# Kernel tuning notes

Hardware: AMD Instinct MI355X
Metric: run time of the kernel (lower is better)

The kernel has to match this reference:

```python
import jax, jax.numpy as jnp
import numpy as np

# dims: V vocab, D embed, C classes, S seq, L layers, M proj_dim (random features), B batch
V, D, C, S, L, M, B = 32000, 512, 2, 2048, 4, 64, 16
H = 4 * D  # FFN hidden


def setup_inputs() -> dict:
    key = jax.random.key(0)
    ks = jax.random.split(key, 16)
    sc = 0.02
    n = lambda k, shape, s=sc: jax.random.normal(k, shape, jnp.float32) * s
    return {
        'x': jax.random.randint(ks[0], (B, S), 0, V),
        'embed': n(ks[1], (V, D)),
        'pos': n(ks[2], (S, D)),
        'Wq': n(ks[3], (L, D, D)), 'bq': jnp.zeros((L, D), jnp.float32),
        'Wk': n(ks[4], (L, D, D)), 'bk': jnp.zeros((L, D), jnp.float32),
        'Wv': n(ks[5], (L, D, D)), 'bv': jnp.zeros((L, D), jnp.float32),
        'P': jax.random.normal(ks[6], (L, D, M), jnp.float32) / np.sqrt(D),  # Performer random-feature projection
        'Wo': n(ks[7], (L, D, D)), 'bo': jnp.zeros((L, D), jnp.float32),
        'ln_g': jnp.ones((L, D), jnp.float32), 'ln_b': jnp.zeros((L, D), jnp.float32),
        'W1': n(ks[8], (L, D, H)), 'b1': jnp.zeros((L, H), jnp.float32),
        'W2': n(ks[9], (L, H, D)), 'b2': jnp.zeros((L, D), jnp.float32),
        'Wc1': n(ks[10], (D, D // 2)), 'bc1': jnp.zeros((D // 2,), jnp.float32),
        'Wc2': n(ks[11], (D // 2, C)), 'bc2': jnp.zeros((C,), jnp.float32),
    }


def _layernorm(x, g, b, eps=1e-5):
    mu = x.mean(-1, keepdims=True)
    var = ((x - mu) ** 2).mean(-1, keepdims=True)
    return (x - mu) * jax.lax.rsqrt(var + eps) * g + b


def reference(x, embed, pos, Wq, bq, Wk, bk, Wv, bv, P, Wo, bo,
              ln_g, ln_b, W1, b1, W2, b2, Wc1, bc1, Wc2, bc2):
    # token embedding + learned positional embedding
    h = embed[x] + pos[None, :, :]  # [B,S,D]
    for l in range(L):
        r = h
        # Performer linear attention
        q = h @ Wq[l] + bq[l]
        k = h @ Wk[l] + bk[l]
        v = h @ Wv[l] + bv[l]
        pq = jax.nn.elu(q @ P[l]) + 1.0  # [B,S,M] positive feature map
        pk = jax.nn.elu(k @ P[l]) + 1.0
        kv = jnp.einsum('bsm,bsd->bmd', pk, v)              # associative K^T V reduction
        z = jnp.einsum('bsm,bm->bs', pq, pk.sum(axis=1)) + 1e-6
        att = jnp.einsum('bsm,bmd->bsd', pq, kv) / z[..., None]
        att = att @ Wo[l] + bo[l]
        # LayerNorm -> FFN (dropout is identity in eval)
        hn = _layernorm(att, ln_g[l], ln_b[l])
        ff = jax.nn.gelu(hn @ W1[l] + b1[l], approximate=False) @ W2[l] + b2[l]
        h = ff + r  # residual around the whole Sequential block
    pooled = h[:, 0, :]  # CLS pooling
    hid = jax.nn.relu(pooled @ Wc1 + bc1)
    return hid @ Wc2 + bc2  # [B,C] logits
```

## Files before the change

kernel.cpp:

```cpp
#include <hip/hip_runtime.h>
#include <hip/hip_bf16.h>
#include <math.h>

constexpr int kV = 32000;
constexpr int kD = 512;
constexpr int kC = 2;
constexpr int kS = 2048;
constexpr int kL = 4;
constexpr int kM = 64;
constexpr int kB = 16;
constexpr int kH = 2048;
constexpr int kBS = kB * kS;

typedef __hip_bfloat16 bf16;
using bf16x8 = __attribute__((ext_vector_type(8))) short;
using f32x4  = __attribute__((ext_vector_type(4))) float;

#define GLOBAL_LOAD_LDS16(gp, lp)                                              \
  __builtin_amdgcn_global_load_lds(                                            \
      (const __attribute__((address_space(1))) void*)(gp),                     \
      (__attribute__((address_space(3))) void*)(lp), 16, 0, 0)

__device__ inline unsigned short f2bf_u16(float f) {
  bf16 b = __float2bfloat16(f);
  return *reinterpret_cast<unsigned short*>(&b);
}

__global__ __launch_bounds__(256) void embed_kernel(const int* __restrict__ x,
    const float* __restrict__ emb, const float* __restrict__ pos,
    float* __restrict__ h, bf16* __restrict__ hb) {
  int tid = blockIdx.x * 256 + threadIdx.x;
  int row = tid >> 7;
  int d4  = tid & 127;
  int tok = x[row];
  int s   = row & (kS - 1);
  float4 e = ((const float4*)emb)[(size_t)tok * 128 + d4];
  float4 p = ((const float4*)pos)[(size_t)s * 128 + d4];
  float4 o;
  o.x = e.x + p.x; o.y = e.y + p.y; o.z = e.z + p.z; o.w = e.w + p.w;
  ((float4*)h)[(size_t)row * 128 + d4] = o;
  ushort4 ub;
  ub.x = f2bf_u16(o.x); ub.y = f2bf_u16(o.y);
  ub.z = f2bf_u16(o.z); ub.w = f2bf_u16(o.w);
  ((ushort4*)hb)[(size_t)row * 128 + d4] = ub;
}

__global__ __launch_bounds__(256) void transpose_cast_kernel(
    const float* __restrict__ W, bf16* __restrict__ Wt, int K, int N,
    size_t zsW, size_t zsWt) {
  __shared__ float tile[32][33];
  W  += zsW  * blockIdx.z;
  Wt += zsWt * blockIdx.z;
  const int k0 = blockIdx.x * 32, n0 = blockIdx.y * 32;
  int tx = threadIdx.x & 31, ty = threadIdx.x >> 5;
#pragma unroll
  for (int i = 0; i < 32; i += 8)
    tile[ty + i][tx] = W[(size_t)(k0 + ty + i) * N + n0 + tx];
  __syncthreads();
#pragma unroll
  for (int i = 0; i < 32; i += 8)
    Wt[(size_t)(n0 + ty + i) * K + k0 + tx] = __float2bfloat16(tile[tx][ty + i]);
}

__global__ __launch_bounds__(256) void cast_bf16_kernel(
    const float* __restrict__ src, bf16* __restrict__ dst) {
  int gid = blockIdx.x * 256 + threadIdx.x;
  float4 v = ((const float4*)src)[gid];
  ushort4 u;
  u.x = f2bf_u16(v.x); u.y = f2bf_u16(v.y);
  u.z = f2bf_u16(v.z); u.w = f2bf_u16(v.w);
  ((ushort4*)dst)[gid] = u;
}

__global__ __launch_bounds__(256) void zero512_kernel(float* __restrict__ p) {
  if (threadIdx.x < 128) ((float4*)p)[threadIdx.x] = make_float4(0.f, 0.f, 0.f, 0.f);
}

__global__ __launch_bounds__(256) void wfold_dual_kernel(
    const float* __restrict__ Wq, const float* __restrict__ Wk,
    const float* __restrict__ P, bf16* __restrict__ Wqpt,
    bf16* __restrict__ Wkpt) {
  int gid = blockIdx.x * 256 + threadIdx.x;
  int l   = gid >> 16;
  int id  = gid & 65535;
  const float* Pl = P + (size_t)l * kD * kM;
  const float* W  = ((id < 32768) ? Wq : Wk) + (size_t)l * kD * kD;
  bf16* out       = ((id < 32768) ? Wqpt : Wkpt) + (size_t)l * kM * kD;
  id &= 32767;
  int m  = id & 63;
  int kk = id >> 6;
  float a0 = 0.f, a1 = 0.f, a2 = 0.f, a3 = 0.f;
#pragma unroll 4
  for (int c = 0; c < kD; c += 4) {
    float4 w = *(const float4*)&W[(size_t)kk * kD + c];
    a0 = fmaf(w.x, Pl[(size_t)(c + 0) * kM + m], a0);
    a1 = fmaf(w.y, Pl[(size_t)(c + 1) * kM + m], a1);
    a2 = fmaf(w.z, Pl[(size_t)(c + 2) * kM + m], a2);
    a3 = fmaf(w.w, Pl[(size_t)(c + 3) * kM + m], a3);
  }
  out[(size_t)m * kD + kk] = __float2bfloat16((a0 + a1) + (a2 + a3));
}

__global__ __launch_bounds__(512) void bfold_kernel(const float* __restrict__ bq,
    const float* __restrict__ bk, const float* __restrict__ P,
    float* __restrict__ bqp, float* __restrict__ bkp) {
  int l = threadIdx.x >> 7;
  int t = threadIdx.x & 127;
  int m = t & (kM - 1);
  const float* Pl  = P + (size_t)l * kD * kM;
  const float* src = ((t >> 6) ? bk : bq) + (size_t)l * kD;
  float* dst       = ((t >> 6) ? bkp : bqp) + (size_t)l * kM;
  float acc = 0.f;
  for (int c = 0; c < kD; ++c) acc += src[c] * Pl[(size_t)c * kM + m];
  dst[m] = acc;
}

__global__ __launch_bounds__(256) void bvwo_kernel(const float* __restrict__ bv,
    const float* __restrict__ Wo, float* __restrict__ bvWo) {
  __shared__ float part[4][64];
  int l = blockIdx.y;
  bv   += (size_t)l * kD;
  Wo   += (size_t)l * kD * kD;
  bvWo += (size_t)l * kD;
  int d0 = blockIdx.x * 64;
  int dc = threadIdx.x & 63;
  int eg = threadIdx.x >> 6;
  float acc = 0.f;
  int e0 = eg * 128;
#pragma unroll 4
  for (int e = e0; e < e0 + 128; ++e)
    acc = fmaf(bv[e], Wo[(size_t)e * kD + d0 + dc], acc);
  part[eg][dc] = acc;
  __syncthreads();
  if (eg == 0)
    bvWo[d0 + dc] = (part[0][dc] + part[1][dc]) + (part[2][dc] + part[3][dc]);
}

template <int BK, int BN, int ACT, bool HAS_RES, bool HAS_OUTER, bool WRITE_F32, bool WRITE_BF16>
__global__ __launch_bounds__(256) void mfma_gemm(
    const bf16* __restrict__ A, const bf16* __restrict__ Wt,
    const float* __restrict__ bias, const float* __restrict__ rowv,
    const float* __restrict__ colv, const float* __restrict__ res,
    float* __restrict__ C, bf16* __restrict__ Cb,
    size_t zsA, size_t zsB, size_t zsC, int K, int N) {
  constexpr int NJ = BN / 32;
  constexpr int CPR = BK / 8;
  constexpr int SW = (BK == 32) ? 1 : 0;
  __shared__ short As[128 * BK];
  __shared__ short Bs[BN * BK];
  A  += zsA * blockIdx.z;
  Wt += zsB * blockIdx.z;
  if (C)  C  += zsC * blockIdx.z;
  if (Cb) Cb += zsC * blockIdx.z;
  const int tid  = threadIdx.x;
  const int lane = tid & 63;
  const int wave = tid >> 6;
  const int nx = gridDim.x;
  const int SH = (gridDim.y & 7) ? gridDim.y : 8;
  const int b_lin = blockIdx.y * nx + blockIdx.x;
  const int stripe = b_lin / (nx * SH);
  const int rem = b_lin - stripe * (nx * SH);
  const int row0 = (stripe * SH + (rem % SH)) * 128;
  const int col0 = (rem / SH) * BN;
  const int wr = (wave & 1) * 64;
  const int wc = (wave >> 1) * (BN / 2);
  const int lcol = lane & 15;
  const int quad = lane >> 4;

  f32x4 acc[4][NJ];
#pragma unroll
  for (int i = 0; i < 4; ++i)
#pragma unroll
    for (int j = 0; j < NJ; ++j) acc[i][j] = (f32x4){0.f, 0.f, 0.f, 0.f};

  for (int k0 = 0; k0 < K; k0 += BK) {
#pragma unroll
    for (int p = 0; p < 128 * CPR / 256; ++p) {
      int idx = p * 256 + tid;
      int r = idx / CPR;
      int kc = (idx % CPR) ^ ((r >> SW) & (CPR - 1));
      GLOBAL_LOAD_LDS16(&A[(size_t)(row0 + r) * K + k0 + kc * 8], &As[idx * 8]);
    }
#pragma unroll
    for (int p = 0; p < BN * CPR / 256; ++p) {
      int idx = p * 256 + tid;
      int r = idx / CPR;
      int kc = (idx % CPR) ^ ((r >> SW) & (CPR - 1));
      GLOBAL_LOAD_LDS16(&Wt[(size_t)(col0 + r) * K + k0 + kc * 8], &Bs[idx * 8]);
    }
    __syncthreads();
#pragma unroll
    for (int kh = 0; kh < BK / 32; ++kh) {
      bf16x8 af[4], bfr[NJ];
#pragma unroll
      for (int i = 0; i < 4; ++i) {
        int rr = wr + i * 16 + lcol;
        int slot = (kh * 4 + quad) ^ ((rr >> SW) & (CPR - 1));
        af[i] = *(const bf16x8*)&As[(rr * CPR + slot) * 8];
      }
#pragma unroll
      for (int j = 0; j < NJ; ++j) {
        int rr = wc + j * 16 + lcol;
        int slot = (kh * 4 + quad) ^ ((rr >> SW) & (CPR - 1));
        bfr[j] = *(const bf16x8*)&Bs[(rr * CPR + slot) * 8];
      }
#pragma unroll
      for (int i = 0; i < 4; ++i)
#pragma unroll
        for (int j = 0; j < NJ; ++j)
          acc[i][j] = __builtin_amdgcn_mfma_f32_16x16x32_bf16(af[i], bfr[j], acc[i][j], 0, 0, 0);
    }
    __syncthreads();
  }

#pragma unroll
  for (int i = 0; i < 4; ++i) {
#pragma unroll
    for (int r = 0; r < 4; ++r) {
      int grow = row0 + wr + i * 16 + quad * 4 + r;
#pragma unroll
      for (int j = 0; j < NJ; ++j) {
        int gcol = col0 + wc + j * 16 + lcol;
        float v = acc[i][j][r];
        if (HAS_OUTER) v += rowv[grow] * colv[gcol];
        else v += bias[gcol];
        if (ACT == 2) v = 0.5f * v * (1.0f + erff(v * 0.70710678118654752f));
        size_t off = (size_t)grow * N + gcol;
        if (HAS_RES) v += res[off];
        if (WRITE_F32) C[off] = v;
        if (WRITE_BF16) Cb[off] = __float2bfloat16(v);
      }
    }
  }
}

template <int ACT, bool HAS_RES, bool WRITE_F32, bool WRITE_BF16>
__global__ __launch_bounds__(512) void mfma_gemm_cnt(
    const bf16* __restrict__ A, const bf16* __restrict__ Wt,
    const float* __restrict__ bias, const float* __restrict__ res,
    float* __restrict__ C, bf16* __restrict__ Cb, int K, int N) {
  constexpr int BK = 64, BN = 128, BM = 128;
  __shared__ short As[2][BM * BK];
  __shared__ short Bs[2][BN * BK];
  const int tid  = threadIdx.x;
  const int lane = tid & 63;
  const int wave = tid >> 6;
  const int nx = gridDim.x;
  const int SH = (gridDim.y & 7) ? gridDim.y : 8;
  const int b_lin = blockIdx.y * nx + blockIdx.x;
  const int stripe = b_lin / (nx * SH);
  const int rem = b_lin - stripe * (nx * SH);
  const int row0 = (stripe * SH + (rem % SH)) * BM;
  const int col0 = (rem / SH) * BN;
  const int wr = (wave & 1) * 64;
  const int wc = (wave >> 1) * 32;
  const int lcol = lane & 15;
  const int quad = lane >> 4;

  f32x4 acc[4][2];
#pragma unroll
  for (int i = 0; i < 4; ++i)
#pragma unroll
    for (int j = 0; j < 2; ++j) acc[i][j] = (f32x4){0.f, 0.f, 0.f, 0.f};

  auto stage = [&](int buf, int k0) {
#pragma unroll
    for (int p = 0; p < 2; ++p) {
      int idx = p * 512 + tid;
      int r = idx >> 3;
      int kc = (idx & 7) ^ (r & 7);
      GLOBAL_LOAD_LDS16(&A[(size_t)(row0 + r) * K + k0 + kc * 8], &As[buf][idx * 8]);
    }
#pragma unroll
    for (int p = 0; p < 2; ++p) {
      int idx = p * 512 + tid;
      int r = idx >> 3;
      int kc = (idx & 7) ^ (r & 7);
      GLOBAL_LOAD_LDS16(&Wt[(size_t)(col0 + r) * K + k0 + kc * 8], &Bs[buf][idx * 8]);
    }
  };

  auto compute = [&](int buf) {
#pragma unroll
    for (int kh = 0; kh < 2; ++kh) {
      bf16x8 af[4], bfr[2];
#pragma unroll
      for (int i = 0; i < 4; ++i) {
        int rr = wr + i * 16 + lcol;
        int slot = (kh * 4 + quad) ^ (rr & 7);
        af[i] = *(const bf16x8*)&As[buf][(rr * 8 + slot) * 8];
      }
#pragma unroll
      for (int j = 0; j < 2; ++j) {
        int rr = wc + j * 16 + lcol;
        int slot = (kh * 4 + quad) ^ (rr & 7);
        bfr[j] = *(const bf16x8*)&Bs[buf][(rr * 8 + slot) * 8];
      }
#pragma unroll
      for (int i = 0; i < 4; ++i)
#pragma unroll
        for (int j = 0; j < 2; ++j)
          acc[i][j] = __builtin_amdgcn_mfma_f32_16x16x32_bf16(af[i], bfr[j], acc[i][j], 0, 0, 0);
    }
  };

  const int NT = K / BK;
  stage(0, 0);
  stage(1, BK);
  for (int t = 0; t < NT - 1; ++t) {
    const int cur = t & 1;
    asm volatile("s_waitcnt vmcnt(4)" ::: "memory");
    __builtin_amdgcn_s_barrier();
    compute(cur);
    __builtin_amdgcn_s_barrier();
    if (t + 2 < NT) stage(cur, (t + 2) * BK);
  }
  asm volatile("s_waitcnt vmcnt(0)" ::: "memory");
  __builtin_amdgcn_s_barrier();
  compute((NT - 1) & 1);

#pragma unroll
  for (int i = 0; i < 4; ++i) {
#pragma unroll
    for (int r = 0; r < 4; ++r) {
      int grow = row0 + wr + i * 16 + quad * 4 + r;
#pragma unroll
      for (int j = 0; j < 2; ++j) {
        int gcol = col0 + wc + j * 16 + lcol;
        float v = acc[i][j][r] + bias[gcol];
        if (ACT == 2) v = 0.5f * v * (1.0f + erff(v * 0.70710678118654752f));
        size_t off = (size_t)grow * N + gcol;
        if (HAS_RES) v += res[off];
        if (WRITE_F32) C[off] = v;
        if (WRITE_BF16) Cb[off] = __float2bfloat16(v);
      }
    }
  }
}

__global__ __launch_bounds__(256) void skinny_dual_gemm(
    const bf16* __restrict__ A, const bf16* __restrict__ Wq,
    const bf16* __restrict__ Wk, const float* __restrict__ bq,
    const float* __restrict__ bk, float* __restrict__ pq,
    float* __restrict__ pk) {
  __shared__ short As[64 * 32];
  __shared__ short Bs[128 * 32];
  const int tid  = threadIdx.x;
  const int lane = tid & 63;
  const int wave = tid >> 6;
  const int row0 = blockIdx.x * 64;
  const int lcol = lane & 15;
  const int quad = lane >> 4;

  f32x4 accq[4], acck[4];
#pragma unroll
  for (int i = 0; i < 4; ++i) {
    accq[i] = (f32x4){0.f, 0.f, 0.f, 0.f};
    acck[i] = (f32x4){0.f, 0.f, 0.f, 0.f};
  }

  for (int k0 = 0; k0 < kD; k0 += 32) {
    {
      int r = tid >> 2;
      int kc = (tid & 3) ^ ((r >> 1) & 3);
      GLOBAL_LOAD_LDS16(&A[(size_t)(row0 + r) * kD + k0 + kc * 8], &As[tid * 8]);
    }
#pragma unroll
    for (int p = 0; p < 2; ++p) {
      int idx = p * 256 + tid;
      int r = idx >> 2;
      int kc = (idx & 3) ^ ((r >> 1) & 3);
      const bf16* src = (r < 64) ? &Wq[(size_t)r * kD + k0 + kc * 8]
                                 : &Wk[(size_t)(r - 64) * kD + k0 + kc * 8];
      GLOBAL_LOAD_LDS16(src, &Bs[idx * 8]);
    }
    __syncthreads();
    bf16x8 af[4], bq_f, bk_f;
#pragma unroll
    for (int i = 0; i < 4; ++i) {
      int rr = i * 16 + lcol;
      af[i] = *(const bf16x8*)&As[(rr * 4 + (quad ^ ((rr >> 1) & 3))) * 8];
    }
    {
      int rr = wave * 16 + lcol;
      bq_f = *(const bf16x8*)&Bs[(rr * 4 + (quad ^ ((rr >> 1) & 3))) * 8];
      int rr2 = 64 + wave * 16 + lcol;
      bk_f = *(const bf16x8*)&Bs[(rr2 * 4 + (quad ^ ((rr2 >> 1) & 3))) * 8];
    }
#pragma unroll
    for (int i = 0; i < 4; ++i) {
      accq[i] = __builtin_amdgcn_mfma_f32_16x16x32_bf16(af[i], bq_f, accq[i], 0, 0, 0);
      acck[i] = __builtin_amdgcn_mfma_f32_16x16x32_bf16(af[i], bk_f, acck[i], 0, 0, 0);
    }
    __syncthreads();
  }

#pragma unroll
  for (int i = 0; i < 4; ++i) {
#pragma unroll
    for (int r = 0; r < 4; ++r) {
      int grow = row0 + i * 16 + quad * 4 + r;
      int gcol = wave * 16 + lcol;
      float vq = accq[i][r] + bq[gcol];
      vq = (vq > 0.f) ? (vq + 1.f) : expf(vq);
      pq[(size_t)grow * kM + gcol] = vq;
      float vk = acck[i][r] + bk[gcol];
      vk = (vk > 0.f) ? (vk + 1.f) : expf(vk);
      pk[(size_t)grow * kM + gcol] = vk;
    }
  }
}

__global__ __launch_bounds__(256) void kvh_split_kernel(const float* __restrict__ pk,
    const bf16* __restrict__ hb, float* __restrict__ part) {
  __shared__ float pkS[16][64];
  __shared__ float vS[16][256];
  const int d0 = blockIdx.x * 256, b = blockIdx.y, split = blockIdx.z;
  const int s_beg = split * 128;
  const float* pkb = pk + (size_t)b * kS * kM;
  const bf16* hbb  = hb + (size_t)b * kS * kD;
  const int tid = threadIdx.x;
  const int tx = tid & 15, ty = tid >> 4;
  float4 acc[4][4];
#pragma unroll
  for (int i = 0; i < 4; ++i)
#pragma unroll
    for (int j = 0; j < 4; ++j) acc[i][j] = make_float4(0.f, 0.f, 0.f, 0.f);

  for (int s0 = s_beg; s0 < s_beg + 128; s0 += 16) {
    {
      int e = tid * 4;
      int sr = e >> 6, mc = e & 63;
      *(float4*)&pkS[sr][mc] = *(const float4*)&pkb[(size_t)(s0 + sr) * kM + mc];
    }
#pragma unroll
    for (int p = 0; p < 2; ++p) {
      int idx = p * 256 + tid;
      int sr = idx >> 5, dc8 = idx & 31;
      uint4 raw = *(const uint4*)&hbb[(size_t)(s0 + sr) * kD + d0 + dc8 * 8];
      float4 f0, f1;
      f0.x = __uint_as_float(raw.x << 16);
      f0.y = __uint_as_float(raw.x & 0xffff0000u);
      f0.z = __uint_as_float(raw.y << 16);
      f0.w = __uint_as_float(raw.y & 0xffff0000u);
      f1.x = __uint_as_float(raw.z << 16);
      f1.y = __uint_as_float(raw.z & 0xffff0000u);
      f1.z = __uint_as_float(raw.w << 16);
      f1.w = __uint_as_float(raw.w & 0xffff0000u);
      *(float4*)&vS[sr][dc8 * 8]     = f0;
      *(float4*)&vS[sr][dc8 * 8 + 4] = f1;
    }
    __syncthreads();
#pragma unroll
    for (int sr = 0; sr < 16; ++sr) {
      float a[4];
#pragma unroll
      for (int i = 0; i < 4; ++i) a[i] = pkS[sr][ty * 4 + i];
      float4 bv4[4];
#pragma unroll
      for (int j = 0; j < 4; ++j) bv4[j] = *(const float4*)&vS[sr][tx * 16 + j * 4];
#pragma unroll
      for (int i = 0; i < 4; ++i)
#pragma unroll
        for (int j = 0; j < 4; ++j) {
          acc[i][j].x += a[i] * bv4[j].x;
          acc[i][j].y += a[i] * bv4[j].y;
          acc[i][j].z += a[i] * bv4[j].z;
          acc[i][j].w += a[i] * bv4[j].w;
        }
    }
    __syncthreads();
  }
  float* pp = part + (((size_t)split * kB + b) * kM) * kD;
#pragma unroll
  for (int i = 0; i < 4; ++i)
#pragma unroll
    for (int j = 0; j < 4; ++j)
      *(float4*)&pp[(size_t)(ty * 4 + i) * kD + d0 + tx * 16 + j * 4] = acc[i][j];
}

__global__ __launch_bounds__(256) void kvh_reduce_kernel(const float* __restrict__ part,
                                                         bf16* __restrict__ kvhb) {
  int gid = blockIdx.x * 256 + threadIdx.x;
  float4 s = make_float4(0.f, 0.f, 0.f, 0.f);
#pragma unroll
  for (int sp = 0; sp < 16; ++sp) {
    float4 p = ((const float4*)part)[(size_t)sp * (kB * kM * kD / 4) + gid];
    s.x += p.x; s.y += p.y; s.z += p.z; s.w += p.w;
  }
  ushort4 u;
  u.x = f2bf_u16(s.x); u.y = f2bf_u16(s.y);
  u.z = f2bf_u16(s.z); u.w = f2bf_u16(s.w);
  ((ushort4*)kvhb)[gid] = u;
}

__global__ __launch_bounds__(256) void zero_pks_kernel(float* __restrict__ p) {
  ((float4*)p)[threadIdx.x] = make_float4(0.f, 0.f, 0.f, 0.f);
}

__global__ __launch_bounds__(256) void pksum_kernel(const float* __restrict__ pk,
                                                    float* __restrict__ pksum) {
  __shared__ float part[4][64];
  int b = blockIdx.x >> 4;
  int split = blockIdx.x & 15;
  int lane = threadIdx.x & 63, w = threadIdx.x >> 6;
  float s = 0.f;
  int base = split * 128 + w * 32;
  for (int i = 0; i < 32; ++i)
    s += pk[((size_t)b * kS + base + i) * kM + lane];
  part[w][lane] = s;
  __syncthreads();
  if (w == 0)
    atomicAdd(&pksum[b * kM + lane],
              part[0][lane] + part[1][lane] + part[2][lane] + part[3][lane]);
}

__global__ __launch_bounds__(256) void att_ln_kernel(
    const float* __restrict__ pq, const float* __restrict__ kvo,
    const float* __restrict__ pks, const float* __restrict__ bo,
    const float* __restrict__ g, const float* __restrict__ bb,
    bf16* __restrict__ out) {
  __shared__ float pqS[32][68];
  __shared__ float kvS[16][520];
  const int s0 = blockIdx.x * 32, b = blockIdx.y;
  const int tid = threadIdx.x;
  const int tx = tid & 15, ty = tid >> 4;

#pragma unroll
  for (int i = 0; i < 2; ++i) {
    int f4 = tid + i * 256;
    int r = f4 >> 4, c = (f4 & 15) * 4;
    *(float4*)&pqS[r][c] = *(const float4*)&pq[((size_t)(b * kS + s0 + r)) * kM + c];
  }

  float4 acc[2][8];
#pragma unroll
  for (int i = 0; i < 2; ++i)
#pragma unroll
    for (int j = 0; j < 8; ++j) acc[i][j] = make_float4(0.f, 0.f, 0.f, 0.f);

  for (int m0 = 0; m0 < kM; m0 += 16) {
#pragma unroll
    for (int p = 0; p < 8; ++p) {
      int idx = p * 256 + tid;
      int sr = idx >> 7, c4 = idx & 127;
      *(float4*)&kvS[sr][c4 * 4] =
          *(const float4*)&kvo[((size_t)b * kM + m0 + sr) * kD + c4 * 4];
    }
    __syncthreads();
#pragma unroll
    for (int mm = 0; mm < 16; ++mm) {
      float a0 = pqS[ty * 2 + 0][m0 + mm];
      float a1 = pqS[ty * 2 + 1][m0 + mm];
#pragma unroll
      for (int j = 0; j < 8; ++j) {
        float4 bv = *(const float4*)&kvS[mm][j * 64 + tx * 4];
        acc[0][j].x += a0 * bv.x; acc[0][j].y += a0 * bv.y;
        acc[0][j].z += a0 * bv.z; acc[0][j].w += a0 * bv.w;
        acc[1][j].x += a1 * bv.x; acc[1][j].y += a1 * bv.y;
        acc[1][j].z += a1 * bv.z; acc[1][j].w += a1 * bv.w;
      }
    }
    __syncthreads();
  }

  float4 pk4 = *(const float4*)&pks[b * kM + tx * 4];
  float z0 = pqS[ty * 2 + 0][tx * 4 + 0] * pk4.x + pqS[ty * 2 + 0][tx * 4 + 1] * pk4.y +
             pqS[ty * 2 + 0][tx * 4 + 2] * pk4.z + pqS[ty * 2 + 0][tx * 4 + 3] * pk4.w;
  float z1 = pqS[ty * 2 + 1][tx * 4 + 0] * pk4.x + pqS[ty * 2 + 1][tx * 4 + 1] * pk4.y +
             pqS[ty * 2 + 1][tx * 4 + 2] * pk4.z + pqS[ty * 2 + 1][tx * 4 + 3] * pk4.w;
  z0 += __shfl_xor(z0, 1); z0 += __shfl_xor(z0, 2);
  z0 += __shfl_xor(z0, 4); z0 += __shfl_xor(z0, 8);
  z1 += __shfl_xor(z1, 1); z1 += __shfl_xor(z1, 2);
  z1 += __shfl_xor(z1, 4); z1 += __shfl_xor(z1, 8);
  float zi0 = 1.0f / (z0 + 1e-6f);
  float zi1 = 1.0f / (z1 + 1e-6f);

#pragma unroll
  for (int j = 0; j < 8; ++j) {
    float4 bo4 = *(const float4*)&bo[j * 64 + tx * 4];
    acc[0][j].x = acc[0][j].x * zi0 + bo4.x; acc[0][j].y = acc[0][j].y * zi0 + bo4.y;
    acc[0][j].z = acc[0][j].z * zi0 + bo4.z; acc[0][j].w = acc[0][j].w * zi0 + bo4.w;
    acc[1][j].x = acc[1][j].x * zi1 + bo4.x; acc[1][j].y = acc[1][j].y * zi1 + bo4.y;
    acc[1][j].z = acc[1][j].z * zi1 + bo4.z; acc[1][j].w = acc[1][j].w * zi1 + bo4.w;
  }

#pragma unroll
  for (int i = 0; i < 2; ++i) {
    float s = 0.f;
#pragma unroll
    for (int j = 0; j < 8; ++j)
      s += (acc[i][j].x + acc[i][j].y) + (acc[i][j].z + acc[i][j].w);
    s += __shfl_xor(s, 1); s += __shfl_xor(s, 2);
    s += __shfl_xor(s, 4); s += __shfl_xor(s, 8);
    float mean = s * (1.0f / kD);
    float v2 = 0.f;
#pragma unroll
    for (int j = 0; j < 8; ++j) {
      float dx = acc[i][j].x - mean, dy = acc[i][j].y - mean;
      float dz = acc[i][j].z - mean, dw = acc[i][j].w - mean;
      v2 += (dx * dx + dy * dy) + (dz * dz + dw * dw);
    }
    v2 += __shfl_xor(v2, 1); v2 += __shfl_xor(v2, 2);
    v2 += __shfl_xor(v2, 4); v2 += __shfl_xor(v2, 8);
    float rstd = rsqrtf(v2 * (1.0f / kD) + 1e-5f);
    size_t rowoff = ((size_t)(b * kS + s0 + ty * 2 + i)) * kD;
#pragma unroll
    for (int j = 0; j < 8; ++j) {
      int col = j * 64 + tx * 4;
      float4 g4 = *(const float4*)&g[col];
      float4 b4 = *(const float4*)&bb[col];
      ushort4 u;
      u.x = f2bf_u16((acc[i][j].x - mean) * rstd * g4.x + b4.x);
      u.y = f2bf_u16((acc[i][j].y - mean) * rstd * g4.y + b4.y);
      u.z = f2bf_u16((acc[i][j].z - mean) * rstd * g4.z + b4.z);
      u.w = f2bf_u16((acc[i][j].w - mean) * rstd * g4.w + b4.w);
      *(ushort4*)&out[rowoff + col] = u;
    }
  }
}

__global__ __launch_bounds__(256) void cls_kernel(const float* __restrict__ h,
    const float* __restrict__ Wc1, const float* __restrict__ bc1,
    const float* __restrict__ Wc2, const float* __restrict__ bc2,
    float* __restrict__ out) {
  __shared__ float r0[4], r1[4];
  int b = blockIdx.x;
  int j = threadIdx.x;
  const float* p = h + (size_t)b * kS * kD;
  float acc = bc1[j];
  for (int i = 0; i < kD; ++i) acc += p[i] * Wc1[i * (kD / 2) + j];
  acc = fmaxf(acc, 0.f);
  float p0 = acc * Wc2[j * kC + 0];
  float p1 = acc * Wc2[j * kC + 1];
#pragma unroll
  for (int off = 32; off; off >>= 1) {
    p0 += __shfl_down(p0, off);
    p1 += __shfl_down(p1, off);
  }
  if ((j & 63) == 0) { r0[j >> 6] = p0; r1[j >> 6] = p1; }
  __syncthreads();
  if (j == 0) {
    out[b * kC + 0] = r0[0] + r0[1] + r0[2] + r0[3] + bc2[0];
    out[b * kC + 1] = r1[0] + r1[1] + r1[2] + r1[3] + bc2[1];
  }
}

extern "C" void kernel_launch(void* const* d_in, const int* in_sizes, int n_in,
                              void* d_out, int out_size, void* d_ws, size_t ws_size,
                              hipStream_t stream) {
  const int*   x    = (const int*)  d_in[0];
  const float* emb  = (const float*)d_in[1];
  const float* pos  = (const float*)d_in[2];
  const float* Wq   = (const float*)d_in[3];
  const float* bq   = (const float*)d_in[4];
  const float* Wk   = (const float*)d_in[5];
  const float* bk   = (const float*)d_in[6];
  const float* Wv   = (const float*)d_in[7];
  const float* bv   = (const float*)d_in[8];
  const float* P    = (const float*)d_in[9];
  const float* Wo   = (const float*)d_in[10];
  const float* bo   = (const float*)d_in[11];
  const float* ln_g = (const float*)d_in[12];
  const float* ln_b = (const float*)d_in[13];
  const float* W1   = (const float*)d_in[14];
  const float* b1   = (const float*)d_in[15];
  const float* W2   = (const float*)d_in[16];
  const float* b2   = (const float*)d_in[17];
  const float* Wc1  = (const float*)d_in[18];
  const float* bc1  = (const float*)d_in[19];
  const float* Wc2  = (const float*)d_in[20];
  const float* bc2  = (const float*)d_in[21];
  float* out = (float*)d_out;

  float* h    = (float*)d_ws;
  float* t0   = h    + (size_t)kBS * kD;
  float* pq   = t0   + (size_t)kBS * kD;
  float* pk   = pq   + (size_t)kBS * kM;
  float* kvo  = pk   + (size_t)kBS * kM;
  float* pks  = kvo  + (size_t)kB * kM * kD;
  float* bqp  = pks  + (size_t)kB * kM;
  float* bkp  = bqp  + (size_t)kL * kM;
  float* bvWo = bkp  + (size_t)kL * kM;
  float* zeros= bvWo + (size_t)kL * kD;
  bf16* hb    = (bf16*)(zeros + kD);
  bf16* ab    = hb + (size_t)kBS * kD;
  bf16* Wqpt  = ab  + (size_t)kBS * kD;
  bf16* Wkpt  = Wqpt + (size_t)kL * kM * kD;
  bf16* Wot   = Wkpt + (size_t)kL * kM * kD;
  bf16* Wvc   = Wot + (size_t)kL * kD * kD;
  bf16* WvWot = Wvc + (size_t)kL * kD * kD;
  bf16* W1t   = WvWot + (size_t)kL * kD * kD;
  bf16* W2t   = W1t + (size_t)kL * kD * kH;
  bf16* kvhb  = W2t + (size_t)kL * kH * kD;
  bf16* F     = (bf16*)t0;
  float* kvpart = (float*)ab;

  zero512_kernel<<<1, 256, 0, stream>>>(zeros);
  embed_kernel<<<kBS * (kD / 4) / 256, 256, 0, stream>>>(x, emb, pos, h, hb);

  wfold_dual_kernel<<<kL * 256, 256, 0, stream>>>(Wq, Wk, P, Wqpt, Wkpt);
  bfold_kernel<<<1, 128 * kL, 0, stream>>>(bq, bk, P, bqp, bkp);
  transpose_cast_kernel<<<dim3(kD / 32, kD / 32, kL), 256, 0, stream>>>(
      Wo, Wot, kD, kD, (size_t)kD * kD, (size_t)kD * kD);
  cast_bf16_kernel<<<kL * kD * kD / 1024, 256, 0, stream>>>(Wv, Wvc);
  mfma_gemm<32, 64, 0, false, false, false, true><<<dim3(8, 4, kL), 256, 0, stream>>>(
      Wot, Wvc, zeros, nullptr, nullptr, nullptr, nullptr, WvWot,
      (size_t)kD * kD, (size_t)kD * kD, (size_t)kD * kD, kD, kD);
  bvwo_kernel<<<dim3(kD / 64, kL), 256, 0, stream>>>(bv, Wo, bvWo);
  transpose_cast_kernel<<<dim3(kD / 32, kH / 32, kL), 256, 0, stream>>>(
      W1, W1t, kD, kH, (size_t)kD * kH, (size_t)kD * kH);
  transpose_cast_kernel<<<dim3(kH / 32, kD / 32, kL), 256, 0, stream>>>(
      W2, W2t, kH, kD, (size_t)kH * kD, (size_t)kH * kD);

  for (int l = 0; l < kL; ++l) {
    skinny_dual_gemm<<<kBS / 64, 256, 0, stream>>>(
        hb, Wqpt + (size_t)l * kM * kD, Wkpt + (size_t)l * kM * kD,
        bqp + (size_t)l * kM, bkp + (size_t)l * kM, pq, pk);
    kvh_split_kernel<<<dim3(kD / 256, kB, 16), 256, 0, stream>>>(pk, hb, kvpart);
    kvh_reduce_kernel<<<kB * kM * kD / 1024, 256, 0, stream>>>(kvpart, kvhb);
    zero_pks_kernel<<<1, 256, 0, stream>>>(pks);
    pksum_kernel<<<kB * 16, 256, 0, stream>>>(pk, pks);
    mfma_gemm<32, 64, 0, false, true, true, false><<<dim3(8, 8), 256, 0, stream>>>(
        kvhb, WvWot + (size_t)l * kD * kD, nullptr, pks, bvWo + (size_t)l * kD,
        nullptr, kvo, nullptr, 0, 0, 0, kD, kD);
    att_ln_kernel<<<dim3(kS / 32, kB), 256, 0, stream>>>(
        pq, kvo, pks, bo + l * kD, ln_g + l * kD, ln_b + l * kD, ab);
    for (int c = 0; c < 2; ++c) {
      size_t ro = (size_t)c * 16384;
      mfma_gemm_cnt<2, false, false, true><<<dim3(kH / 128, 16384 / 128), 512, 0, stream>>>(
          ab + ro * kD, W1t + (size_t)l * kD * kH, b1 + l * kH, nullptr, nullptr, F, kD, kH);
      mfma_gemm_cnt<0, true, true, true><<<dim3(kD / 128, 16384 / 128), 512, 0, stream>>>(
          F, W2t + (size_t)l * kH * kD, b2 + l * kD, h + ro * kD, h + ro * kD, hb + ro * kD, kH, kD);
    }
  }

  cls_kernel<<<kB, 256, 0, stream>>>(h, Wc1, bc1, Wc2, bc2, out);
}
```

Baseline: 1.501 ms.

## Double-buffer skinny dual GEMM and fold pk column sums into kv split kernel

The skinny Q/K feature GEMM now uses two LDS buffers with async global-to-LDS loads, so the next K-tile is prefetched while the current one is computed. The separate pksum kernel is removed: the kv split kernel accumulates pk column sums from the pk tile it already loads (only in x-block 0) and adds them atomically. The number of sequence splits also drops from 16 to 8, which halves the partial buffer traffic and reduction work but gives fewer blocks and longer per-block loops. The vmcnt(3) wait count assumes exactly three outstanding loads per stage.

```diff
diff --git a/kernel.cpp b/kernel.cpp
--- a/kernel.cpp
+++ b/kernel.cpp
@@ -11,6 +11,7 @@
 constexpr int kB = 16;
 constexpr int kH = 2048;
 constexpr int kBS = kB * kS;
+constexpr int kSplits = 8;
 
 typedef __hip_bfloat16 bf16;
 using bf16x8 = __attribute__((ext_vector_type(8))) short;
@@ -343,8 +344,8 @@
     const bf16* __restrict__ Wk, const float* __restrict__ bq,
     const float* __restrict__ bk, float* __restrict__ pq,
     float* __restrict__ pk) {
-  __shared__ short As[64 * 32];
-  __shared__ short Bs[128 * 32];
+  __shared__ short As[2][64 * 32];
+  __shared__ short Bs[2][128 * 32];
   const int tid  = threadIdx.x;
   const int lane = tid & 63;
   const int wave = tid >> 6;
@@ -359,11 +360,11 @@
     acck[i] = (f32x4){0.f, 0.f, 0.f, 0.f};
   }
 
-  for (int k0 = 0; k0 < kD; k0 += 32) {
+  auto stage = [&](int buf, int k0) {
     {
       int r = tid >> 2;
       int kc = (tid & 3) ^ ((r >> 1) & 3);
-      GLOBAL_LOAD_LDS16(&A[(size_t)(row0 + r) * kD + k0 + kc * 8], &As[tid * 8]);
+      GLOBAL_LOAD_LDS16(&A[(size_t)(row0 + r) * kD + k0 + kc * 8], &As[buf][tid * 8]);
     }
 #pragma unroll
     for (int p = 0; p < 2; ++p) {
@@ -372,28 +373,44 @@
       int kc = (idx & 3) ^ ((r >> 1) & 3);
       const bf16* src = (r < 64) ? &Wq[(size_t)r * kD + k0 + kc * 8]
                                  : &Wk[(size_t)(r - 64) * kD + k0 + kc * 8];
-      GLOBAL_LOAD_LDS16(src, &Bs[idx * 8]);
-    }
-    __syncthreads();
+      GLOBAL_LOAD_LDS16(src, &Bs[buf][idx * 8]);
+    }
+  };
+
+  auto compute = [&](int buf) {
     bf16x8 af[4], bq_f, bk_f;
 #pragma unroll
     for (int i = 0; i < 4; ++i) {
       int rr = i * 16 + lcol;
-      af[i] = *(const bf16x8*)&As[(rr * 4 + (quad ^ ((rr >> 1) & 3))) * 8];
+      af[i] = *(const bf16x8*)&As[buf][(rr * 4 + (quad ^ ((rr >> 1) & 3))) * 8];
     }
     {
       int rr = wave * 16 + lcol;
-      bq_f = *(const bf16x8*)&Bs[(rr * 4 + (quad ^ ((rr >> 1) & 3))) * 8];
+      bq_f = *(const bf16x8*)&Bs[buf][(rr * 4 + (quad ^ ((rr >> 1) & 3))) * 8];
       int rr2 = 64 + wave * 16 + lcol;
-      bk_f = *(const bf16x8*)&Bs[(rr2 * 4 + (quad ^ ((rr2 >> 1) & 3))) * 8];
+      bk_f = *(const bf16x8*)&Bs[buf][(rr2 * 4 + (quad ^ ((rr2 >> 1) & 3))) * 8];
     }
 #pragma unroll
     for (int i = 0; i < 4; ++i) {
       accq[i] = __builtin_amdgcn_mfma_f32_16x16x32_bf16(af[i], bq_f, accq[i], 0, 0, 0);
       acck[i] = __builtin_amdgcn_mfma_f32_16x16x32_bf16(af[i], bk_f, acck[i], 0, 0, 0);
     }
-    __syncthreads();
-  }
+  };
+
+  const int NT = kD / 32;
+  stage(0, 0);
+  stage(1, 32);
+  for (int t = 0; t < NT - 1; ++t) {
+    const int cur = t & 1;
+    asm volatile("s_waitcnt vmcnt(3)" ::: "memory");
+    __builtin_amdgcn_s_barrier();
+    compute(cur);
+    __builtin_amdgcn_s_barrier();
+    if (t + 2 < NT) stage(cur, (t + 2) * 32);
+  }
+  asm volatile("s_waitcnt vmcnt(0)" ::: "memory");
+  __builtin_amdgcn_s_barrier();
+  compute((NT - 1) & 1);
 
 #pragma unroll
   for (int i = 0; i < 4; ++i) {
@@ -412,26 +429,31 @@
 }
 
 __global__ __launch_bounds__(256) void kvh_split_kernel(const float* __restrict__ pk,
-    const bf16* __restrict__ hb, float* __restrict__ part) {
+    const bf16* __restrict__ hb, float* __restrict__ part,
+    float* __restrict__ pks) {
   __shared__ float pkS[16][64];
   __shared__ float vS[16][256];
   const int d0 = blockIdx.x * 256, b = blockIdx.y, split = blockIdx.z;
-  const int s_beg = split * 128;
+  const int s_beg = split * (kS / kSplits);
   const float* pkb = pk + (size_t)b * kS * kM;
   const bf16* hbb  = hb + (size_t)b * kS * kD;
   const int tid = threadIdx.x;
   const int tx = tid & 15, ty = tid >> 4;
+  const bool do_pks = (blockIdx.x == 0);
+  float lsum0 = 0.f, lsum1 = 0.f, lsum2 = 0.f, lsum3 = 0.f;
+  const int mc = (tid * 4) & 63;
   float4 acc[4][4];
 #pragma unroll
   for (int i = 0; i < 4; ++i)
 #pragma unroll
     for (int j = 0; j < 4; ++j) acc[i][j] = make_float4(0.f, 0.f, 0.f, 0.f);
 
-  for (int s0 = s_beg; s0 < s_beg + 128; s0 += 16) {
+  for (int s0 = s_beg; s0 < s_beg + kS / kSplits; s0 += 16) {
     {
-      int e = tid * 4;
-      int sr = e >> 6, mc = e & 63;
-      *(float4*)&pkS[sr][mc] = *(const float4*)&pkb[(size_t)(s0 + sr) * kM + mc];
+      int sr = tid >> 4;
+      float4 v = *(const float4*)&pkb[(size_t)(s0 + sr) * kM + mc];
+      *(float4*)&pkS[sr][mc] = v;
+      if (do_pks) { lsum0 += v.x; lsum1 += v.y; lsum2 += v.z; lsum3 += v.w; }
     }
 #pragma unroll
     for (int p = 0; p < 2; ++p) {
@@ -471,6 +493,12 @@
     }
     __syncthreads();
   }
+  if (do_pks) {
+    atomicAdd(&pks[b * kM + mc + 0], lsum0);
+    atomicAdd(&pks[b * kM + mc + 1], lsum1);
+    atomicAdd(&pks[b * kM + mc + 2], lsum2);
+    atomicAdd(&pks[b * kM + mc + 3], lsum3);
+  }
   float* pp = part + (((size_t)split * kB + b) * kM) * kD;
 #pragma unroll
   for (int i = 0; i < 4; ++i)
@@ -484,7 +512,7 @@
   int gid = blockIdx.x * 256 + threadIdx.x;
   float4 s = make_float4(0.f, 0.f, 0.f, 0.f);
 #pragma unroll
-  for (int sp = 0; sp < 16; ++sp) {
+  for (int sp = 0; sp < kSplits; ++sp) {
     float4 p = ((const float4*)part)[(size_t)sp * (kB * kM * kD / 4) + gid];
     s.x += p.x; s.y += p.y; s.z += p.z; s.w += p.w;
   }
@@ -496,23 +524,6 @@
 
 __global__ __launch_bounds__(256) void zero_pks_kernel(float* __restrict__ p) {
   ((float4*)p)[threadIdx.x] = make_float4(0.f, 0.f, 0.f, 0.f);
-}
-
-__global__ __launch_bounds__(256) void pksum_kernel(const float* __restrict__ pk,
-                                                    float* __restrict__ pksum) {
-  __shared__ float part[4][64];
-  int b = blockIdx.x >> 4;
-  int split = blockIdx.x & 15;
-  int lane = threadIdx.x & 63, w = threadIdx.x >> 6;
-  float s = 0.f;
-  int base = split * 128 + w * 32;
-  for (int i = 0; i < 32; ++i)
-    s += pk[((size_t)b * kS + base + i) * kM + lane];
-  part[w][lane] = s;
-  __syncthreads();
-  if (w == 0)
-    atomicAdd(&pksum[b * kM + lane],
-              part[0][lane] + part[1][lane] + part[2][lane] + part[3][lane]);
 }
 
 __global__ __launch_bounds__(256) void att_ln_kernel(
@@ -717,10 +728,9 @@
     skinny_dual_gemm<<<kBS / 64, 256, 0, stream>>>(
         hb, Wqpt + (size_t)l * kM * kD, Wkpt + (size_t)l * kM * kD,
         bqp + (size_t)l * kM, bkp + (size_t)l * kM, pq, pk);
-    kvh_split_kernel<<<dim3(kD / 256, kB, 16), 256, 0, stream>>>(pk, hb, kvpart);
+    zero_pks_kernel<<<1, 256, 0, stream>>>(pks);
+    kvh_split_kernel<<<dim3(kD / 256, kB, kSplits), 256, 0, stream>>>(pk, hb, kvpart, pks);
     kvh_reduce_kernel<<<kB * kM * kD / 1024, 256, 0, stream>>>(kvpart, kvhb);
-    zero_pks_kernel<<<1, 256, 0, stream>>>(pks);
-    pksum_kernel<<<kB * 16, 256, 0, stream>>>(pk, pks);
     mfma_gemm<32, 64, 0, false, true, true, false><<<dim3(8, 8), 256, 0, stream>>>(
         kvhb, WvWot + (size_t)l * kD * kD, nullptr, pks, bvWo + (size_t)l * kD,
         nullptr, kvo, nullptr, 0, 0, 0, kD, kD);
```

New measurement: 1.540 ms. 1.03x slower.
